# Kernel tuning notes

Hardware: AMD Instinct MI355X
Metric: run time of the kernel (lower is better)

Reference implementation:

```python
import jax, jax.numpy as jnp
import numpy as np

N, E, F_IN, H1, H2, C, K, G = 50000, 800000, 64, 64, 128, 2, 5, 64


def setup_inputs() -> dict:
    key = jax.random.key(0)
    ks = jax.random.split(key, 12)
    x = jax.random.normal(ks[0], (N, F_IN), dtype=jnp.float32)
    edge_index = jax.random.randint(ks[1], (2, E), 0, N, dtype=jnp.int64)
    edge_attr = jax.random.uniform(ks[2], (E,), dtype=jnp.float32)
    batch = jnp.sort(jax.random.randint(ks[3], (N,), 0, G, dtype=jnp.int64))
    def glorot(k, shape, fan_in):
        return jax.random.normal(k, shape, dtype=jnp.float32) * (1.0 / np.sqrt(fan_in))
    # ChebConv weights: [K, in, out]
    W1 = glorot(ks[4], (K, F_IN, H1), F_IN)
    b1 = jnp.zeros((H1,), jnp.float32)
    W2 = glorot(ks[5], (K, H1, H1), H1)
    b2 = jnp.zeros((H1,), jnp.float32)
    W3 = glorot(ks[6], (K, H1, H2), H1)
    b3 = jnp.zeros((H2,), jnp.float32)
    Wl = glorot(ks[7], (H2, C), H2)
    bl = jnp.zeros((C,), jnp.float32)
    return {"x": x, "edge_index": edge_index, "edge_attr": edge_attr, "batch": batch,
            "W1": W1, "b1": b1, "W2": W2, "b2": b2, "W3": W3, "b3": b3, "Wl": Wl, "bl": bl}


def _cheb_norm(edge_index, edge_attr, num_nodes):
    # sym-normalized scaled Laplacian L_hat = 2L/lambda_max - I with lambda_max=2:
    # off-diagonal weights -D^{-1/2} A D^{-1/2}; diagonal is exactly 0.
    src = edge_index[0]
    dst = edge_index[1]
    deg = jax.ops.segment_sum(edge_attr, src, num_segments=num_nodes)
    dis = jnp.where(deg > 0, jax.lax.rsqrt(deg), 0.0)
    norm = -dis[src] * edge_attr * dis[dst]
    return src, dst, norm


def _cheb_conv(x, src, dst, norm, W, b):
    # out = sum_k T_k(L_hat) x @ W[k], Chebyshev recurrence T_k = 2 L_hat T_{k-1} - T_{k-2}
    num_nodes = x.shape[0]
    def prop(z):  # L_hat @ z via edge gather-scale-scatter
        return jax.ops.segment_sum(norm[:, None] * z[src], dst, num_segments=num_nodes)
    Kk = W.shape[0]
    Tx0 = x
    out = Tx0 @ W[0]
    if Kk > 1:
        Tx1 = prop(Tx0)
        out = out + Tx1 @ W[1]
        for k in range(2, Kk):
            Tx2 = 2.0 * prop(Tx1) - Tx0
            out = out + Tx2 @ W[k]
            Tx0, Tx1 = Tx1, Tx2
    return out + b


def reference(x, edge_index, edge_attr, batch, W1, b1, W2, b2, W3, b3, Wl, bl):
    num_nodes = x.shape[0]
    src, dst, norm = _cheb_norm(edge_index, edge_attr, num_nodes)
    h = jax.nn.relu(_cheb_conv(x, src, dst, norm, W1, b1))
    h = jax.nn.relu(_cheb_conv(h, src, dst, norm, W2, b2))
    h = jax.nn.relu(_cheb_conv(h, src, dst, norm, W3, b3))
    # global mean pool over graph segment ids
    sums = jax.ops.segment_sum(h, batch, num_segments=G)
    cnt = jax.ops.segment_sum(jnp.ones((num_nodes,), h.dtype), batch, num_segments=G)
    hg = sums / jnp.maximum(cnt, 1.0)[:, None]
    out = hg @ Wl + bl
    return (out, hg)
```

## Files before the change

kernel.cpp:

```cpp
#include <hip/hip_runtime.h>
#include <hip/hip_fp16.h>


constexpr int F = 64;
constexpr int H2C = 128;
constexpr int GG = 64;
constexpr int CC = 2;
constexpr int KT = 5;
constexpr int PP = 16;

typedef __attribute__((ext_vector_type(8))) short short8v;
typedef __attribute__((ext_vector_type(4))) float f32x4;
typedef unsigned short ushortT;
typedef __attribute__((ext_vector_type(4))) unsigned short u16x4;
typedef __attribute__((ext_vector_type(8))) unsigned short u16x8;

__device__ inline ushortT f2bf(float f) {
  unsigned u = __float_as_uint(f);
  u = (u + 0x7fffu + ((u >> 16) & 1u)) >> 16;
  return (ushortT)u;
}
__device__ inline float bf2f(ushortT u) {
  return __uint_as_float((unsigned)u << 16);
}
__device__ inline float h2f_bits(unsigned short b) {
  __half_raw hr; hr.x = b;
  return __half2float(*reinterpret_cast<__half*>(&hr));
}
__device__ inline unsigned short f2h_bits(float v) {
  __half h = __float2half(v);
  return reinterpret_cast<__half_raw*>(&h)->x;
}


__global__ void pre_hist(const int* __restrict__ ei, const float* __restrict__ attr,
                         float* __restrict__ deg, int* __restrict__ cnt,
                         ushortT* __restrict__ rankr, int E) {
  int e = blockIdx.x * 256 + threadIdx.x;
  if (e < E) {
    atomicAdd(&deg[ei[e]], attr[e]);
    int rk = atomicAdd(&cnt[ei[E + e]], 1);
    rankr[e] = (ushortT)rk;
  }
}

__global__ void dis_k(const float* __restrict__ deg, float* __restrict__ dis, int n) {
  int i = blockIdx.x * 256 + threadIdx.x;
  if (i < n) { float d = deg[i]; dis[i] = d > 0.f ? rsqrtf(d) : 0.f; }
}


__global__ __launch_bounds__(256) void scan_a(const int* __restrict__ cnt,
                                              int* __restrict__ bsum, int n) {
  int t = threadIdx.x, lane = t & 63, w = t >> 6;
  int base = blockIdx.x * 1024 + t * 4;
  int s = 0;
#pragma unroll
  for (int j = 0; j < 4; ++j) { int i = base + j; if (i < n) s += cnt[i]; }
#pragma unroll
  for (int d = 1; d < 64; d <<= 1) s += __shfl_down(s, d, 64);
  __shared__ int ws[4];
  if (lane == 0) ws[w] = s;
  __syncthreads();
  if (t == 0) bsum[blockIdx.x] = ws[0] + ws[1] + ws[2] + ws[3];
}

__global__ void scan_b(int* __restrict__ bsum, int nb) {
  if (threadIdx.x == 0) {
    int acc = 0;
    for (int i = 0; i < nb; ++i) { acc += bsum[i]; bsum[i] = acc; }
  }
}

__global__ __launch_bounds__(256) void scan_c(const int* __restrict__ cnt,
                                              const int* __restrict__ bscan,
                                              int* __restrict__ off, int n) {
  int b = blockIdx.x, t = threadIdx.x;
  int lane = t & 63, w = t >> 6;
  int idx = b * 1024 + t * 4;
  int v[4];
#pragma unroll
  for (int j = 0; j < 4; ++j) { int i = idx + j; v[j] = (i < n) ? cnt[i] : 0; }
  int s1 = v[0], s2 = s1 + v[1], s3 = s2 + v[2], s4 = s3 + v[3];
  int x = s4;
#pragma unroll
  for (int d = 1; d < 64; d <<= 1) { int y = __shfl_up(x, d, 64); if (lane >= d) x += y; }
  __shared__ int wtot[4];
  if (lane == 63) wtot[w] = x;
  __syncthreads();
  int wbase = 0;
  for (int i = 0; i < w; ++i) wbase += wtot[i];
  int base = ((b > 0) ? bscan[b - 1] : 0) + wbase + (x - s4);
  if (idx + 0 < n) off[idx + 1] = base + s1;
  if (idx + 1 < n) off[idx + 2] = base + s2;
  if (idx + 2 < n) off[idx + 3] = base + s3;
  if (idx + 3 < n) off[idx + 4] = base + s4;
  if (b == 0 && t == 0) off[0] = 0;
}

__global__ void scatter_k(const int* __restrict__ ei, const float* __restrict__ attr,
                          const float* __restrict__ dis,
                          const ushortT* __restrict__ rankr,
                          const int* __restrict__ off, unsigned* __restrict__ ep4,
                          int E) {
  int e = blockIdx.x * 256 + threadIdx.x;
  if (e < E) {
    int s = ei[e], d = ei[E + e];
    int pos = off[d] + (int)rankr[e];
    float nv = -dis[s] * attr[e] * dis[d];
    ep4[pos] = ((unsigned)f2h_bits(nv) << 16) | (unsigned)(s & 0xFFFF);
  }
}

__global__ void cvt_k(const float* __restrict__ x, ushortT* __restrict__ o, int n4) {
  int i = blockIdx.x * 256 + threadIdx.x;
  if (i < n4) {
    float4 v = ((const float4*)x)[i];
    u16x4 r = {f2bf(v.x), f2bf(v.y), f2bf(v.z), f2bf(v.w)};
    ((u16x4*)o)[i] = r;
  }
}


__global__ __launch_bounds__(256) void prop_k(const ushortT* __restrict__ z,
                                              const int* __restrict__ off,
                                              const unsigned* __restrict__ ep4,
                                              const float* __restrict__ TprevF,
                                              const ushortT* __restrict__ TprevB,
                                              ushortT* __restrict__ out_bf, int n) {
  int wid = (blockIdx.x * 256 + threadIdx.x) >> 6;
  int lane = threadIdx.x & 63;
  if (wid >= n) return;
  int s = off[wid], e = off[wid + 1];
  int sub = lane & 7;
  int t = lane >> 3;
  float acc[8];
#pragma unroll
  for (int c = 0; c < 8; ++c) acc[c] = 0.f;
  for (int base = s; base < e; base += 64) {
    int idx = base + lane;
    unsigned m = (idx < e) ? ep4[idx] : 0u;
    int cntc = min(64, e - base);
    for (int j = 0; j < cntc; j += 16) {
      unsigned me0 = (unsigned)__shfl((int)m, j + t, 64);
      unsigned me1 = (unsigned)__shfl((int)m, j + 8 + t, 64);
      float w0 = h2f_bits((unsigned short)(me0 >> 16));
      float w1 = h2f_bits((unsigned short)(me1 >> 16));
      int s0 = (int)(me0 & 0xFFFF);
      int s1 = (int)(me1 & 0xFFFF);
      u16x8 v0 = *(const u16x8*)(z + ((size_t)s0 << 6) + sub * 8);
      u16x8 v1 = *(const u16x8*)(z + ((size_t)s1 << 6) + sub * 8);
#pragma unroll
      for (int c = 0; c < 8; ++c) acc[c] = fmaf(w0, bf2f(v0[c]), acc[c]);
#pragma unroll
      for (int c = 0; c < 8; ++c) acc[c] = fmaf(w1, bf2f(v1[c]), acc[c]);
    }
  }
#pragma unroll
  for (int c = 0; c < 8; ++c) {
    float v = acc[c];
    v += __shfl_xor(v, 8, 64);
    v += __shfl_xor(v, 16, 64);
    v += __shfl_xor(v, 32, 64);
    acc[c] = v;
  }
  if (lane < 8) {
    size_t oi = ((size_t)wid << 6) + (size_t)lane * 8;
    float r[8];
    if (TprevF) {
      const float4* tp = (const float4*)(TprevF + oi);
      float4 t0 = tp[0], t1 = tp[1];
      r[0] = 2.f * acc[0] - t0.x; r[1] = 2.f * acc[1] - t0.y;
      r[2] = 2.f * acc[2] - t0.z; r[3] = 2.f * acc[3] - t0.w;
      r[4] = 2.f * acc[4] - t1.x; r[5] = 2.f * acc[5] - t1.y;
      r[6] = 2.f * acc[6] - t1.z; r[7] = 2.f * acc[7] - t1.w;
    } else if (TprevB) {
      u16x8 tp = *(const u16x8*)(TprevB + oi);
#pragma unroll
      for (int c = 0; c < 8; ++c) r[c] = 2.f * acc[c] - bf2f(tp[c]);
    } else {
#pragma unroll
      for (int c = 0; c < 8; ++c) r[c] = acc[c];
    }
    u16x8 o;
#pragma unroll
    for (int c = 0; c < 8; ++c) o[c] = f2bf(r[c]);
    *(u16x8*)(out_bf + oi) = o;
  }
}


__global__ void repack_k(const float* __restrict__ W, ushortT* __restrict__ Bp, int H) {
  int t = blockIdx.x * 256 + threadIdx.x;
  int lane = t & 63, fid = t >> 6;
  int CT = H / 16;
  int nf = KT * 2 * CT;
  if (fid >= nf) return;
  int ct = fid % CT;
  int ks = (fid / CT) & 1;
  int term = fid / (CT * 2);
  int nn = ct * 16 + (lane & 15);
  int kb = ks * 32 + (lane >> 4) * 8;
  short8v out;
#pragma unroll
  for (int e = 0; e < 8; ++e)
    out[e] = (short)f2bf(W[((size_t)term * F + kb + e) * H + nn]);
  ((short8v*)Bp)[(size_t)fid * 64 + lane] = out;
}


template <int H>
__global__ __launch_bounds__(256) void gemm5_mfma(const ushortT* __restrict__ T0,
                                                  const ushortT* __restrict__ T1,
                                                  const ushortT* __restrict__ T2,
                                                  const ushortT* __restrict__ T3,
                                                  const ushortT* __restrict__ T4,
                                                  const ushortT* __restrict__ Bp,
                                                  const float* __restrict__ bias,
                                                  ushortT* __restrict__ Y, int n) {
  constexpr int CT = H / 16;
  int wave = threadIdx.x >> 6;
  int lane = threadIdx.x & 63;
  int rbase = blockIdx.x * 64 + wave * 16;
  int arow = rbase + (lane & 15);
  if (arow > n - 1) arow = n - 1;
  const short8v* bp = (const short8v*)Bp;
  const ushortT* Ts[5] = {T0, T1, T2, T3, T4};

  f32x4 acc[CT];
#pragma unroll
  for (int c = 0; c < CT; ++c) acc[c] = (f32x4){0.f, 0.f, 0.f, 0.f};

#pragma unroll
  for (int term = 0; term < KT; ++term) {
    const ushortT* T = Ts[term];
#pragma unroll
    for (int ks = 0; ks < 2; ++ks) {
      int kb = ks * 32 + (lane >> 4) * 8;
      short8v af = *(const short8v*)(T + (size_t)arow * F + kb);
      int fid0 = (term * 2 + ks) * CT;
#pragma unroll
      for (int ct = 0; ct < CT; ++ct) {
        short8v bf = bp[(size_t)(fid0 + ct) * 64 + lane];
        acc[ct] = __builtin_amdgcn_mfma_f32_16x16x32_bf16(af, bf, acc[ct], 0, 0, 0);
      }
    }
  }
  int col0 = lane & 15;
  int rrow = rbase + (lane >> 4) * 4;
#pragma unroll
  for (int ct = 0; ct < CT; ++ct) {
    int col = ct * 16 + col0;
    float bv = bias[col];
#pragma unroll
    for (int i = 0; i < 4; ++i) {
      int gr = rrow + i;
      if (gr < n) Y[(size_t)gr * H + col] = f2bf(fmaxf(acc[ct][i] + bv, 0.f));
    }
  }
}


__global__ void gbounds_k(const int* __restrict__ batch, int* __restrict__ gstart, int n) {
  int g = threadIdx.x;
  if (g > GG) return;
  int lo = 0, hi = n;
  while (lo < hi) {
    int mid = (lo + hi) >> 1;
    if (batch[mid] < g) lo = mid + 1; else hi = mid;
  }
  gstart[g] = lo;
}

__global__ __launch_bounds__(256) void pool1_k(const ushortT* __restrict__ h,
                                               const int* __restrict__ gstart,
                                               float* __restrict__ partials) {
  int g = blockIdx.x / PP, p = blockIdx.x % PP;
  int s = gstart[g], e = gstart[g + 1];
  int len = e - s;
  int ss = s + (int)((long long)len * p / PP);
  int se = s + (int)((long long)len * (p + 1) / PP);
  int tid = threadIdx.x;
  int c = tid & (H2C - 1), half = tid >> 7;
  float acc = 0.f;
  for (int i = ss + half; i < se; i += 2)
    acc += bf2f(h[(size_t)i * H2C + c]);
  __shared__ float sums[2][H2C];
  sums[half][c] = acc;
  __syncthreads();
  if (tid < H2C)
    partials[(size_t)blockIdx.x * H2C + tid] = sums[0][tid] + sums[1][tid];
}

__global__ __launch_bounds__(128) void pool2_k(const float* __restrict__ partials,
                                               const int* __restrict__ gstart,
                                               const float* __restrict__ Wl,
                                               const float* __restrict__ bl,
                                               float* __restrict__ outp) {
  int g = blockIdx.x, tid = threadIdx.x;
  float s = 0.f;
  for (int p = 0; p < PP; ++p) s += partials[(size_t)(g * PP + p) * H2C + tid];
  float cntv = fmaxf((float)(gstart[g + 1] - gstart[g]), 1.f);
  float hg = s / cntv;
  outp[GG * CC + g * H2C + tid] = hg;
  __shared__ float red[2][H2C];
  red[0][tid] = hg * Wl[tid * CC + 0];
  red[1][tid] = hg * Wl[tid * CC + 1];
  __syncthreads();
  for (int st = 64; st > 0; st >>= 1) {
    if (tid < st) { red[0][tid] += red[0][tid + st]; red[1][tid] += red[1][tid + st]; }
    __syncthreads();
  }
  if (tid == 0) {
    outp[g * CC + 0] = red[0][0] + bl[0];
    outp[g * CC + 1] = red[1][0] + bl[1];
  }
}


extern "C" void kernel_launch(void* const* d_in, const int* in_sizes, int n_in,
                              void* d_out, int out_size, void* d_ws, size_t ws_size,
                              hipStream_t stream) {
  const float* x    = (const float*)d_in[0];
  const int*   ei   = (const int*)d_in[1];
  const float* attr = (const float*)d_in[2];
  const int*   batch= (const int*)d_in[3];
  const float* W1 = (const float*)d_in[4];
  const float* b1 = (const float*)d_in[5];
  const float* W2 = (const float*)d_in[6];
  const float* b2 = (const float*)d_in[7];
  const float* W3 = (const float*)d_in[8];
  const float* b3 = (const float*)d_in[9];
  const float* Wl = (const float*)d_in[10];
  const float* bl = (const float*)d_in[11];
  float* outp = (float*)d_out;

  const int N = in_sizes[3];
  const int E = in_sizes[2];

  char* p = (char*)d_ws;
  auto alloc = [&](size_t bytes) {
    char* r = p;
    p += (bytes + 255) & ~(size_t)255;
    return r;
  };
  float* deg   = (float*)alloc((size_t)N * 4);
  int*   cnt   = (int*)alloc((size_t)N * 4);
  float* dis   = (float*)alloc((size_t)N * 4);
  int*   off   = (int*)alloc((size_t)(N + 1) * 4);
  ushortT* rankr = (ushortT*)alloc((size_t)E * 2);
  unsigned* ep4 = (unsigned*)alloc((size_t)E * 4);
  int*   bsum  = (int*)alloc(4096);
  int*   gstart= (int*)alloc((size_t)(GG + 1) * 4);
  ushortT* Bp1 = (ushortT*)alloc((size_t)KT * 2 * 4 * 64 * 8 * 2);
  ushortT* Bp2 = (ushortT*)alloc((size_t)KT * 2 * 4 * 64 * 8 * 2);
  ushortT* Bp3 = (ushortT*)alloc((size_t)KT * 2 * 8 * 64 * 8 * 2);
  ushortT* X0  = (ushortT*)alloc((size_t)N * F * 2);
  ushortT* Abf = (ushortT*)alloc((size_t)N * F * 2);
  ushortT* Bbf = (ushortT*)alloc((size_t)N * F * 2);
  ushortT* Cbf = (ushortT*)alloc((size_t)N * F * 2);
  ushortT* Dbf = (ushortT*)alloc((size_t)N * F * 2);
  ushortT* Y1  = (ushortT*)alloc((size_t)N * F * 2);
  ushortT* Y2  = (ushortT*)alloc((size_t)N * F * 2);
  ushortT* Y3  = (ushortT*)alloc((size_t)N * H2C * 2);
  float* partials = (float*)alloc((size_t)GG * PP * H2C * 4);

  hipMemsetAsync(deg, 0, (size_t)N * 4, stream);
  hipMemsetAsync(cnt, 0, (size_t)N * 4, stream);

  int eb = (E + 255) / 256;
  int nb = (N + 255) / 256;
  int sb = (N + 1023) / 1024;

  repack_k<<<(KT * 2 * 4 * 64 + 255) / 256, 256, 0, stream>>>(W1, Bp1, 64);
  repack_k<<<(KT * 2 * 4 * 64 + 255) / 256, 256, 0, stream>>>(W2, Bp2, 64);
  repack_k<<<(KT * 2 * 8 * 64 + 255) / 256, 256, 0, stream>>>(W3, Bp3, 128);
  cvt_k<<<((N * F / 4) + 255) / 256, 256, 0, stream>>>(x, X0, N * F / 4);

  pre_hist<<<eb, 256, 0, stream>>>(ei, attr, deg, cnt, rankr, E);
  dis_k<<<nb, 256, 0, stream>>>(deg, dis, N);
  scan_a<<<sb, 256, 0, stream>>>(cnt, bsum, N);
  scan_b<<<1, 64, 0, stream>>>(bsum, sb);
  scan_c<<<sb, 256, 0, stream>>>(cnt, bsum, off, N);
  scatter_k<<<eb, 256, 0, stream>>>(ei, attr, dis, rankr, off, ep4, E);
  gbounds_k<<<1, 128, 0, stream>>>(batch, gstart, N);

  int pb = (N + 3) / 4;
  auto prop = [&](const ushortT* z, const float* TprevF, const ushortT* TprevB,
                  ushortT* obf) {
    prop_k<<<pb, 256, 0, stream>>>(z, off, ep4, TprevF, TprevB, obf, N);
  };

  auto run_layer = [&](const ushortT* T0, const float* T0f, const ushortT* Bpk,
                       const float* bk, ushortT* Yout, int Hout) {
    prop(T0, nullptr, nullptr, Abf);
    prop(Abf, T0f, T0f ? nullptr : T0, Bbf);
    prop(Bbf, nullptr, Abf, Cbf);
    prop(Cbf, nullptr, Bbf, Dbf);
    if (Hout == 64)
      gemm5_mfma<64><<<(N + 63) / 64, 256, 0, stream>>>(T0, Abf, Bbf, Cbf, Dbf,
                                                        Bpk, bk, Yout, N);
    else
      gemm5_mfma<128><<<(N + 63) / 64, 256, 0, stream>>>(T0, Abf, Bbf, Cbf, Dbf,
                                                         Bpk, bk, Yout, N);
  };

  run_layer(X0, x,       Bp1, b1, Y1, 64);
  run_layer(Y1, nullptr, Bp2, b2, Y2, 64);
  run_layer(Y2, nullptr, Bp3, b3, Y3, 128);

  pool1_k<<<GG * PP, 256, 0, stream>>>(Y3, gstart, partials);
  pool2_k<<<GG, 128, 0, stream>>>(partials, gstart, Wl, bl, outp);
}
```

Before: 452.9 us.

## Process four nodes per wave in prop with prefetched edge lists; hoist GEMM A loads

Result: no change. 453.9 us (+0.2%).

```diff
diff --git a/kernel.cpp b/kernel.cpp
--- a/kernel.cpp
+++ b/kernel.cpp
@@ -128,64 +128,89 @@
                                               const float* __restrict__ TprevF,
                                               const ushortT* __restrict__ TprevB,
                                               ushortT* __restrict__ out_bf, int n) {
-  int wid = (blockIdx.x * 256 + threadIdx.x) >> 6;
+  int wv = (blockIdx.x * 256 + threadIdx.x) >> 6;
   int lane = threadIdx.x & 63;
-  if (wid >= n) return;
-  int s = off[wid], e = off[wid + 1];
+  int n0 = wv * 4;
+  if (n0 >= n) return;
   int sub = lane & 7;
   int t = lane >> 3;
-  float acc[8];
-#pragma unroll
-  for (int c = 0; c < 8; ++c) acc[c] = 0.f;
-  for (int base = s; base < e; base += 64) {
-    int idx = base + lane;
-    unsigned m = (idx < e) ? ep4[idx] : 0u;
-    int cntc = min(64, e - base);
-    for (int j = 0; j < cntc; j += 16) {
-      unsigned me0 = (unsigned)__shfl((int)m, j + t, 64);
-      unsigned me1 = (unsigned)__shfl((int)m, j + 8 + t, 64);
-      float w0 = h2f_bits((unsigned short)(me0 >> 16));
-      float w1 = h2f_bits((unsigned short)(me1 >> 16));
-      int s0 = (int)(me0 & 0xFFFF);
-      int s1 = (int)(me1 & 0xFFFF);
-      u16x8 v0 = *(const u16x8*)(z + ((size_t)s0 << 6) + sub * 8);
-      u16x8 v1 = *(const u16x8*)(z + ((size_t)s1 << 6) + sub * 8);
-#pragma unroll
-      for (int c = 0; c < 8; ++c) acc[c] = fmaf(w0, bf2f(v0[c]), acc[c]);
-#pragma unroll
-      for (int c = 0; c < 8; ++c) acc[c] = fmaf(w1, bf2f(v1[c]), acc[c]);
-    }
-  }
-#pragma unroll
-  for (int c = 0; c < 8; ++c) {
-    float v = acc[c];
-    v += __shfl_xor(v, 8, 64);
-    v += __shfl_xor(v, 16, 64);
-    v += __shfl_xor(v, 32, 64);
-    acc[c] = v;
-  }
-  if (lane < 8) {
-    size_t oi = ((size_t)wid << 6) + (size_t)lane * 8;
-    float r[8];
-    if (TprevF) {
-      const float4* tp = (const float4*)(TprevF + oi);
-      float4 t0 = tp[0], t1 = tp[1];
-      r[0] = 2.f * acc[0] - t0.x; r[1] = 2.f * acc[1] - t0.y;
-      r[2] = 2.f * acc[2] - t0.z; r[3] = 2.f * acc[3] - t0.w;
-      r[4] = 2.f * acc[4] - t1.x; r[5] = 2.f * acc[5] - t1.y;
-      r[6] = 2.f * acc[6] - t1.z; r[7] = 2.f * acc[7] - t1.w;
-    } else if (TprevB) {
-      u16x8 tp = *(const u16x8*)(TprevB + oi);
-#pragma unroll
-      for (int c = 0; c < 8; ++c) r[c] = 2.f * acc[c] - bf2f(tp[c]);
-    } else {
-#pragma unroll
-      for (int c = 0; c < 8; ++c) r[c] = acc[c];
-    }
-    u16x8 o;
-#pragma unroll
-    for (int c = 0; c < 8; ++c) o[c] = f2bf(r[c]);
-    *(u16x8*)(out_bf + oi) = o;
+  int offv = 0;
+  {
+    int oi = n0 + lane;
+    if (lane <= 4 && oi <= n) offv = off[oi];
+  }
+  int s_i = __builtin_amdgcn_readlane(offv, 0);
+  int e_i = __builtin_amdgcn_readlane(offv, 1);
+  unsigned m_cur = (s_i + lane < e_i) ? ep4[s_i + lane] : 0u;
+
+#pragma unroll
+  for (int i = 0; i < 4; ++i) {
+    int nd = n0 + i;
+    if (nd >= n) break;
+    int s = s_i, e = e_i;
+    int s_n = 0, e_n = 0;
+    unsigned m_next = 0u;
+    if (i < 3) {
+      s_n = __builtin_amdgcn_readlane(offv, i + 1);
+      e_n = __builtin_amdgcn_readlane(offv, i + 2);
+      m_next = (s_n + lane < e_n) ? ep4[s_n + lane] : 0u;
+    }
+    float acc[8];
+#pragma unroll
+    for (int c = 0; c < 8; ++c) acc[c] = 0.f;
+    unsigned m = m_cur;
+    int base = s;
+    while (base < e) {
+      int cntc = min(64, e - base);
+      for (int j = 0; j < cntc; j += 16) {
+        unsigned me0 = (unsigned)__shfl((int)m, j + t, 64);
+        unsigned me1 = (unsigned)__shfl((int)m, j + 8 + t, 64);
+        float w0 = h2f_bits((unsigned short)(me0 >> 16));
+        float w1 = h2f_bits((unsigned short)(me1 >> 16));
+        int s0 = (int)(me0 & 0xFFFF);
+        int s1 = (int)(me1 & 0xFFFF);
+        u16x8 v0 = *(const u16x8*)(z + ((size_t)s0 << 6) + sub * 8);
+        u16x8 v1 = *(const u16x8*)(z + ((size_t)s1 << 6) + sub * 8);
+#pragma unroll
+        for (int c = 0; c < 8; ++c) acc[c] = fmaf(w0, bf2f(v0[c]), acc[c]);
+#pragma unroll
+        for (int c = 0; c < 8; ++c) acc[c] = fmaf(w1, bf2f(v1[c]), acc[c]);
+      }
+      base += 64;
+      if (base < e) m = (base + lane < e) ? ep4[base + lane] : 0u;
+    }
+#pragma unroll
+    for (int c = 0; c < 8; ++c) {
+      float v = acc[c];
+      v += __shfl_xor(v, 8, 64);
+      v += __shfl_xor(v, 16, 64);
+      v += __shfl_xor(v, 32, 64);
+      acc[c] = v;
+    }
+    if (lane < 8) {
+      size_t oi = ((size_t)nd << 6) + (size_t)lane * 8;
+      float r[8];
+      if (TprevF) {
+        const float4* tp = (const float4*)(TprevF + oi);
+        float4 t0 = tp[0], t1 = tp[1];
+        r[0] = 2.f * acc[0] - t0.x; r[1] = 2.f * acc[1] - t0.y;
+        r[2] = 2.f * acc[2] - t0.z; r[3] = 2.f * acc[3] - t0.w;
+        r[4] = 2.f * acc[4] - t1.x; r[5] = 2.f * acc[5] - t1.y;
+        r[6] = 2.f * acc[6] - t1.z; r[7] = 2.f * acc[7] - t1.w;
+      } else if (TprevB) {
+        u16x8 tp = *(const u16x8*)(TprevB + oi);
+#pragma unroll
+        for (int c = 0; c < 8; ++c) r[c] = 2.f * acc[c] - bf2f(tp[c]);
+      } else {
+#pragma unroll
+        for (int c = 0; c < 8; ++c) r[c] = acc[c];
+      }
+      u16x8 o;
+#pragma unroll
+      for (int c = 0; c < 8; ++c) o[c] = f2bf(r[c]);
+      *(u16x8*)(out_bf + oi) = o;
+    }
+    s_i = s_n; e_i = e_n; m_cur = m_next;
   }
 }
 
@@ -226,24 +251,27 @@
   if (arow > n - 1) arow = n - 1;
   const short8v* bp = (const short8v*)Bp;
   const ushortT* Ts[5] = {T0, T1, T2, T3, T4};
-
-  f32x4 acc[CT];
-#pragma unroll
-  for (int c = 0; c < CT; ++c) acc[c] = (f32x4){0.f, 0.f, 0.f, 0.f};
-
+  int kb = (lane >> 4) * 8;
+
+  short8v afr[10];
 #pragma unroll
   for (int term = 0; term < KT; ++term) {
     const ushortT* T = Ts[term];
-#pragma unroll
-    for (int ks = 0; ks < 2; ++ks) {
-      int kb = ks * 32 + (lane >> 4) * 8;
-      short8v af = *(const short8v*)(T + (size_t)arow * F + kb);
-      int fid0 = (term * 2 + ks) * CT;
-#pragma unroll
-      for (int ct = 0; ct < CT; ++ct) {
-        short8v bf = bp[(size_t)(fid0 + ct) * 64 + lane];
-        acc[ct] = __builtin_amdgcn_mfma_f32_16x16x32_bf16(af, bf, acc[ct], 0, 0, 0);
-      }
+    afr[term * 2 + 0] = *(const short8v*)(T + (size_t)arow * F + kb);
+    afr[term * 2 + 1] = *(const short8v*)(T + (size_t)arow * F + 32 + kb);
+  }
+
+  f32x4 acc[CT];
+#pragma unroll
+  for (int c = 0; c < CT; ++c) acc[c] = (f32x4){0.f, 0.f, 0.f, 0.f};
+
+#pragma unroll
+  for (int f = 0; f < KT * 2; ++f) {
+    short8v af = afr[f];
+#pragma unroll
+    for (int ct = 0; ct < CT; ++ct) {
+      short8v bf = bp[(size_t)(f * CT + ct) * 64 + lane];
+      acc[ct] = __builtin_amdgcn_mfma_f32_16x16x32_bf16(af, bf, acc[ct], 0, 0, 0);
     }
   }
   int col0 = lane & 15;
@@ -385,7 +413,7 @@
   scatter_k<<<eb, 256, 0, stream>>>(ei, attr, dis, rankr, off, ep4, E);
   gbounds_k<<<1, 128, 0, stream>>>(batch, gstart, N);
 
-  int pb = (N + 3) / 4;
+  int pb = (N + 15) / 16;
   auto prop = [&](const ushortT* z, const float* TprevF, const ushortT* TprevB,
                   ushortT* obf) {
     prop_k<<<pb, 256, 0, stream>>>(z, off, ep4, TprevF, TprevB, obf, N);
```

## Split feature matrices into two 32-column planes for cache-friendly propagation

Applied to the files above, without the earlier changes.

After: 654.3 us. 44.5% more time.

```diff
diff --git a/kernel.cpp b/kernel.cpp
--- a/kernel.cpp
+++ b/kernel.cpp
@@ -112,28 +112,42 @@
   }
 }
 
-__global__ void cvt_k(const float* __restrict__ x, ushortT* __restrict__ o, int n4) {
+__global__ void cvt_k(const float* __restrict__ x, ushortT* __restrict__ oa,
+                      ushortT* __restrict__ ob, int n) {
   int i = blockIdx.x * 256 + threadIdx.x;
-  if (i < n4) {
+  if (i < n * 16) {
+    int row = i >> 4;
+    int c4 = (i & 15) * 4;
     float4 v = ((const float4*)x)[i];
     u16x4 r = {f2bf(v.x), f2bf(v.y), f2bf(v.z), f2bf(v.w)};
-    ((u16x4*)o)[i] = r;
-  }
-}
-
-
-__global__ __launch_bounds__(256) void prop_k(const ushortT* __restrict__ z,
+    ushortT* dst = (c4 >= 32 ? ob : oa) + (size_t)row * 32 + (c4 & 31);
+    *(u16x4*)dst = r;
+  }
+}
+
+
+__global__ __launch_bounds__(256) void prop_k(const ushortT* __restrict__ z0,
+                                              const ushortT* __restrict__ z1,
                                               const int* __restrict__ off,
                                               const unsigned* __restrict__ ep4,
                                               const float* __restrict__ TprevF,
-                                              const ushortT* __restrict__ TprevB,
-                                              ushortT* __restrict__ out_bf, int n) {
-  int wid = (blockIdx.x * 256 + threadIdx.x) >> 6;
+                                              const ushortT* __restrict__ tb0,
+                                              const ushortT* __restrict__ tb1,
+                                              ushortT* __restrict__ o0,
+                                              ushortT* __restrict__ o1, int n) {
+  int bid = blockIdx.x;
+  int half = (bid >> 2) & 1;
+  int tile = (bid >> 3) * 4 + (bid & 3);
+  int wave = threadIdx.x >> 6;
   int lane = threadIdx.x & 63;
-  if (wid >= n) return;
-  int s = off[wid], e = off[wid + 1];
-  int sub = lane & 7;
-  int t = lane >> 3;
+  int nd = tile * 4 + wave;
+  if (nd >= n) return;
+  const ushortT* z = half ? z1 : z0;
+  const ushortT* tb = half ? tb1 : tb0;
+  ushortT* op = half ? o1 : o0;
+  int sub = lane & 3;
+  int t = lane >> 2;
+  int s = off[nd], e = off[nd + 1];
   float acc[8];
 #pragma unroll
   for (int c = 0; c < 8; ++c) acc[c] = 0.f;
@@ -142,40 +156,35 @@
     unsigned m = (idx < e) ? ep4[idx] : 0u;
     int cntc = min(64, e - base);
     for (int j = 0; j < cntc; j += 16) {
-      unsigned me0 = (unsigned)__shfl((int)m, j + t, 64);
-      unsigned me1 = (unsigned)__shfl((int)m, j + 8 + t, 64);
-      float w0 = h2f_bits((unsigned short)(me0 >> 16));
-      float w1 = h2f_bits((unsigned short)(me1 >> 16));
-      int s0 = (int)(me0 & 0xFFFF);
-      int s1 = (int)(me1 & 0xFFFF);
-      u16x8 v0 = *(const u16x8*)(z + ((size_t)s0 << 6) + sub * 8);
-      u16x8 v1 = *(const u16x8*)(z + ((size_t)s1 << 6) + sub * 8);
-#pragma unroll
-      for (int c = 0; c < 8; ++c) acc[c] = fmaf(w0, bf2f(v0[c]), acc[c]);
-#pragma unroll
-      for (int c = 0; c < 8; ++c) acc[c] = fmaf(w1, bf2f(v1[c]), acc[c]);
+      unsigned me = (unsigned)__shfl((int)m, j + t, 64);
+      float w = h2f_bits((unsigned short)(me >> 16));
+      int src = (int)(me & 0xFFFF);
+      u16x8 v = *(const u16x8*)(z + ((size_t)src << 5) + sub * 8);
+#pragma unroll
+      for (int c = 0; c < 8; ++c) acc[c] = fmaf(w, bf2f(v[c]), acc[c]);
     }
   }
 #pragma unroll
   for (int c = 0; c < 8; ++c) {
     float v = acc[c];
+    v += __shfl_xor(v, 4, 64);
     v += __shfl_xor(v, 8, 64);
     v += __shfl_xor(v, 16, 64);
     v += __shfl_xor(v, 32, 64);
     acc[c] = v;
   }
-  if (lane < 8) {
-    size_t oi = ((size_t)wid << 6) + (size_t)lane * 8;
+  if (lane < 4) {
+    size_t oi = ((size_t)nd << 5) + (size_t)lane * 8;
     float r[8];
     if (TprevF) {
-      const float4* tp = (const float4*)(TprevF + oi);
+      const float4* tp = (const float4*)(TprevF + ((size_t)nd << 6) + half * 32 + lane * 8);
       float4 t0 = tp[0], t1 = tp[1];
       r[0] = 2.f * acc[0] - t0.x; r[1] = 2.f * acc[1] - t0.y;
       r[2] = 2.f * acc[2] - t0.z; r[3] = 2.f * acc[3] - t0.w;
       r[4] = 2.f * acc[4] - t1.x; r[5] = 2.f * acc[5] - t1.y;
       r[6] = 2.f * acc[6] - t1.z; r[7] = 2.f * acc[7] - t1.w;
-    } else if (TprevB) {
-      u16x8 tp = *(const u16x8*)(TprevB + oi);
+    } else if (tb) {
+      u16x8 tp = *(const u16x8*)(tb + oi);
 #pragma unroll
       for (int c = 0; c < 8; ++c) r[c] = 2.f * acc[c] - bf2f(tp[c]);
     } else {
@@ -185,7 +194,7 @@
     u16x8 o;
 #pragma unroll
     for (int c = 0; c < 8; ++c) o[c] = f2bf(r[c]);
-    *(u16x8*)(out_bf + oi) = o;
+    *(u16x8*)(op + oi) = o;
   }
 }
 
@@ -210,14 +219,14 @@
 
 
 template <int H>
-__global__ __launch_bounds__(256) void gemm5_mfma(const ushortT* __restrict__ T0,
-                                                  const ushortT* __restrict__ T1,
-                                                  const ushortT* __restrict__ T2,
-                                                  const ushortT* __restrict__ T3,
-                                                  const ushortT* __restrict__ T4,
-                                                  const ushortT* __restrict__ Bp,
-                                                  const float* __restrict__ bias,
-                                                  ushortT* __restrict__ Y, int n) {
+__global__ __launch_bounds__(256) void gemm5_mfma(
+    const ushortT* __restrict__ T0a, const ushortT* __restrict__ T0b,
+    const ushortT* __restrict__ T1a, const ushortT* __restrict__ T1b,
+    const ushortT* __restrict__ T2a, const ushortT* __restrict__ T2b,
+    const ushortT* __restrict__ T3a, const ushortT* __restrict__ T3b,
+    const ushortT* __restrict__ T4a, const ushortT* __restrict__ T4b,
+    const ushortT* __restrict__ Bp, const float* __restrict__ bias,
+    ushortT* __restrict__ Ya, ushortT* __restrict__ Yb, int n) {
   constexpr int CT = H / 16;
   int wave = threadIdx.x >> 6;
   int lane = threadIdx.x & 63;
@@ -225,25 +234,28 @@
   int arow = rbase + (lane & 15);
   if (arow > n - 1) arow = n - 1;
   const short8v* bp = (const short8v*)Bp;
-  const ushortT* Ts[5] = {T0, T1, T2, T3, T4};
+  const ushortT* Tsa[5] = {T0a, T1a, T2a, T3a, T4a};
+  const ushortT* Tsb[5] = {T0b, T1b, T2b, T3b, T4b};
+  int kb8 = (lane >> 4) * 8;
+
+  short8v afr[10];
+#pragma unroll
+  for (int term = 0; term < KT; ++term) {
+    afr[term * 2 + 0] = *(const short8v*)(Tsa[term] + ((size_t)arow << 5) + kb8);
+    afr[term * 2 + 1] = *(const short8v*)(Tsb[term] + ((size_t)arow << 5) + kb8);
+  }
 
   f32x4 acc[CT];
 #pragma unroll
   for (int c = 0; c < CT; ++c) acc[c] = (f32x4){0.f, 0.f, 0.f, 0.f};
 
 #pragma unroll
-  for (int term = 0; term < KT; ++term) {
-    const ushortT* T = Ts[term];
-#pragma unroll
-    for (int ks = 0; ks < 2; ++ks) {
-      int kb = ks * 32 + (lane >> 4) * 8;
-      short8v af = *(const short8v*)(T + (size_t)arow * F + kb);
-      int fid0 = (term * 2 + ks) * CT;
-#pragma unroll
-      for (int ct = 0; ct < CT; ++ct) {
-        short8v bf = bp[(size_t)(fid0 + ct) * 64 + lane];
-        acc[ct] = __builtin_amdgcn_mfma_f32_16x16x32_bf16(af, bf, acc[ct], 0, 0, 0);
-      }
+  for (int f = 0; f < KT * 2; ++f) {
+    short8v af = afr[f];
+#pragma unroll
+    for (int ct = 0; ct < CT; ++ct) {
+      short8v bf = bp[(size_t)(f * CT + ct) * 64 + lane];
+      acc[ct] = __builtin_amdgcn_mfma_f32_16x16x32_bf16(af, bf, acc[ct], 0, 0, 0);
     }
   }
   int col0 = lane & 15;
@@ -255,7 +267,15 @@
 #pragma unroll
     for (int i = 0; i < 4; ++i) {
       int gr = rrow + i;
-      if (gr < n) Y[(size_t)gr * H + col] = f2bf(fmaxf(acc[ct][i] + bv, 0.f));
+      if (gr < n) {
+        ushortT v = f2bf(fmaxf(acc[ct][i] + bv, 0.f));
+        if (H == 128) {
+          Ya[(size_t)gr * H + col] = v;
+        } else {
+          ushortT* dst = (col >= 32 ? Yb : Ya);
+          dst[((size_t)gr << 5) + (col & 31)] = v;
+        }
+      }
     }
   }
 }
@@ -355,18 +375,19 @@
   ushortT* Bp1 = (ushortT*)alloc((size_t)KT * 2 * 4 * 64 * 8 * 2);
   ushortT* Bp2 = (ushortT*)alloc((size_t)KT * 2 * 4 * 64 * 8 * 2);
   ushortT* Bp3 = (ushortT*)alloc((size_t)KT * 2 * 8 * 64 * 8 * 2);
-  ushortT* X0  = (ushortT*)alloc((size_t)N * F * 2);
-  ushortT* Abf = (ushortT*)alloc((size_t)N * F * 2);
-  ushortT* Bbf = (ushortT*)alloc((size_t)N * F * 2);
-  ushortT* Cbf = (ushortT*)alloc((size_t)N * F * 2);
-  ushortT* Dbf = (ushortT*)alloc((size_t)N * F * 2);
-  ushortT* Y1  = (ushortT*)alloc((size_t)N * F * 2);
-  ushortT* Y2  = (ushortT*)alloc((size_t)N * F * 2);
+  size_t plane = (size_t)N * 32;
+  ushortT* X0a = (ushortT*)alloc(plane * 2); ushortT* X0b = (ushortT*)alloc(plane * 2);
+  ushortT* Aa  = (ushortT*)alloc(plane * 2); ushortT* Ab  = (ushortT*)alloc(plane * 2);
+  ushortT* Ba  = (ushortT*)alloc(plane * 2); ushortT* Bb  = (ushortT*)alloc(plane * 2);
+  ushortT* Ca  = (ushortT*)alloc(plane * 2); ushortT* Cb  = (ushortT*)alloc(plane * 2);
+  ushortT* Da  = (ushortT*)alloc(plane * 2); ushortT* Db  = (ushortT*)alloc(plane * 2);
+  ushortT* Y1a = (ushortT*)alloc(plane * 2); ushortT* Y1b = (ushortT*)alloc(plane * 2);
+  ushortT* Y2a = (ushortT*)alloc(plane * 2); ushortT* Y2b = (ushortT*)alloc(plane * 2);
   ushortT* Y3  = (ushortT*)alloc((size_t)N * H2C * 2);
   float* partials = (float*)alloc((size_t)GG * PP * H2C * 4);
 
-  hipMemsetAsync(deg, 0, (size_t)N * 4, stream);
-  hipMemsetAsync(cnt, 0, (size_t)N * 4, stream);
+  size_t degPad = ((size_t)N * 4 + 255) & ~(size_t)255;
+  hipMemsetAsync(deg, 0, degPad + (size_t)N * 4, stream);
 
   int eb = (E + 255) / 256;
   int nb = (N + 255) / 256;
@@ -375,7 +396,7 @@
   repack_k<<<(KT * 2 * 4 * 64 + 255) / 256, 256, 0, stream>>>(W1, Bp1, 64);
   repack_k<<<(KT * 2 * 4 * 64 + 255) / 256, 256, 0, stream>>>(W2, Bp2, 64);
   repack_k<<<(KT * 2 * 8 * 64 + 255) / 256, 256, 0, stream>>>(W3, Bp3, 128);
-  cvt_k<<<((N * F / 4) + 255) / 256, 256, 0, stream>>>(x, X0, N * F / 4);
+  cvt_k<<<((N * 16) + 255) / 256, 256, 0, stream>>>(x, X0a, X0b, N);
 
   pre_hist<<<eb, 256, 0, stream>>>(ei, attr, deg, cnt, rankr, E);
   dis_k<<<nb, 256, 0, stream>>>(deg, dis, N);
@@ -385,29 +406,33 @@
   scatter_k<<<eb, 256, 0, stream>>>(ei, attr, dis, rankr, off, ep4, E);
   gbounds_k<<<1, 128, 0, stream>>>(batch, gstart, N);
 
-  int pb = (N + 3) / 4;
-  auto prop = [&](const ushortT* z, const float* TprevF, const ushortT* TprevB,
-                  ushortT* obf) {
-    prop_k<<<pb, 256, 0, stream>>>(z, off, ep4, TprevF, TprevB, obf, N);
+  int ntiles = (N + 3) / 4;
+  int ntp = ((ntiles + 3) / 4) * 4;
+  int pgrid = 2 * ntp;
+  auto prop = [&](const ushortT* za, const ushortT* zb, const float* TprevF,
+                  const ushortT* tba, const ushortT* tbb,
+                  ushortT* oa, ushortT* ob) {
+    prop_k<<<pgrid, 256, 0, stream>>>(za, zb, off, ep4, TprevF, tba, tbb, oa, ob, N);
   };
 
-  auto run_layer = [&](const ushortT* T0, const float* T0f, const ushortT* Bpk,
-                       const float* bk, ushortT* Yout, int Hout) {
-    prop(T0, nullptr, nullptr, Abf);
-    prop(Abf, T0f, T0f ? nullptr : T0, Bbf);
-    prop(Bbf, nullptr, Abf, Cbf);
-    prop(Cbf, nullptr, Bbf, Dbf);
+  auto run_layer = [&](const ushortT* T0a, const ushortT* T0b, const float* T0f,
+                       const ushortT* Bpk, const float* bk,
+                       ushortT* Yla, ushortT* Ylb, int Hout) {
+    prop(T0a, T0b, nullptr, nullptr, nullptr, Aa, Ab);
+    prop(Aa, Ab, T0f, T0f ? nullptr : T0a, T0f ? nullptr : T0b, Ba, Bb);
+    prop(Ba, Bb, nullptr, Aa, Ab, Ca, Cb);
+    prop(Ca, Cb, nullptr, Ba, Bb, Da, Db);
     if (Hout == 64)
-      gemm5_mfma<64><<<(N + 63) / 64, 256, 0, stream>>>(T0, Abf, Bbf, Cbf, Dbf,
-                                                        Bpk, bk, Yout, N);
+      gemm5_mfma<64><<<(N + 63) / 64, 256, 0, stream>>>(
+          T0a, T0b, Aa, Ab, Ba, Bb, Ca, Cb, Da, Db, Bpk, bk, Yla, Ylb, N);
     else
-      gemm5_mfma<128><<<(N + 63) / 64, 256, 0, stream>>>(T0, Abf, Bbf, Cbf, Dbf,
-                                                         Bpk, bk, Yout, N);
+      gemm5_mfma<128><<<(N + 63) / 64, 256, 0, stream>>>(
+          T0a, T0b, Aa, Ab, Ba, Bb, Ca, Cb, Da, Db, Bpk, bk, Yla, nullptr, N);
   };
 
-  run_layer(X0, x,       Bp1, b1, Y1, 64);
-  run_layer(Y1, nullptr, Bp2, b2, Y2, 64);
-  run_layer(Y2, nullptr, Bp3, b3, Y3, 128);
+  run_layer(X0a, X0b, x,       Bp1, b1, Y1a, Y1b, 64);
+  run_layer(Y1a, Y1b, nullptr, Bp2, b2, Y2a, Y2b, 64);
+  run_layer(Y2a, Y2b, nullptr, Bp3, b3, Y3, nullptr, 128);
 
   pool1_k<<<GG * PP, 256, 0, stream>>>(Y3, gstart, partials);
   pool2_k<<<GG, 128, 0, stream>>>(partials, gstart, Wl, bl, outp);
```

## Replace global-atomic degree histogram with per-block packed LDS histograms and merge

Applied to the files above, without the earlier changes.

Result: no change. 453.1 us (+0.0%).

```diff
diff --git a/kernel.cpp b/kernel.cpp
--- a/kernel.cpp
+++ b/kernel.cpp
@@ -8,6 +8,9 @@
 constexpr int CC = 2;
 constexpr int KT = 5;
 constexpr int PP = 16;
+constexpr int EPB = 8192;
+constexpr int NQ = 12500;
+constexpr int QW = NQ / 2;
 
 typedef __attribute__((ext_vector_type(8))) short short8v;
 typedef __attribute__((ext_vector_type(4))) float f32x4;
@@ -33,20 +36,68 @@
 }
 
 
-__global__ void pre_hist(const int* __restrict__ ei, const float* __restrict__ attr,
-                         float* __restrict__ deg, int* __restrict__ cnt,
-                         ushortT* __restrict__ rankr, int E) {
-  int e = blockIdx.x * 256 + threadIdx.x;
-  if (e < E) {
-    atomicAdd(&deg[ei[e]], attr[e]);
-    int rk = atomicAdd(&cnt[ei[E + e]], 1);
-    rankr[e] = (ushortT)rk;
-  }
-}
-
-__global__ void dis_k(const float* __restrict__ deg, float* __restrict__ dis, int n) {
-  int i = blockIdx.x * 256 + threadIdx.x;
-  if (i < n) { float d = deg[i]; dis[i] = d > 0.f ? rsqrtf(d) : 0.f; }
+__global__ __launch_bounds__(256) void hist_k(const int* __restrict__ ei,
+                                              const float* __restrict__ attr,
+                                              unsigned* __restrict__ degP,
+                                              unsigned* __restrict__ cntP,
+                                              ushortT* __restrict__ lrank, int E) {
+  __shared__ unsigned hd[QW];
+  __shared__ unsigned hc[QW];
+  int blk = blockIdx.x, tid = threadIdx.x;
+  int e0 = blk * EPB;
+#pragma unroll 1
+  for (int q = 0; q < 4; ++q) {
+    int nbase = q * NQ;
+    for (int i = tid; i < QW; i += 256) { hd[i] = 0u; hc[i] = 0u; }
+    __syncthreads();
+    for (int i = tid; i < EPB; i += 256) {
+      int e = e0 + i;
+      if (e < E) {
+        int s = ei[e], d = ei[E + e];
+        if ((unsigned)(s - nbase) < (unsigned)NQ) {
+          unsigned fv = (unsigned)__float2uint_rn(attr[e] * 512.f);
+          int sl = s - nbase;
+          atomicAdd(&hd[sl >> 1], fv << (16 * (sl & 1)));
+        }
+        if ((unsigned)(d - nbase) < (unsigned)NQ) {
+          int dl = d - nbase;
+          unsigned old = atomicAdd(&hc[dl >> 1], 1u << (16 * (dl & 1)));
+          lrank[e] = (ushortT)((old >> (16 * (dl & 1))) & 0xFFFFu);
+        }
+      }
+    }
+    __syncthreads();
+    for (int i = tid; i < QW; i += 256) {
+      degP[(size_t)blk * (4 * QW) + q * QW + i] = hd[i];
+      cntP[(size_t)blk * (4 * QW) + q * QW + i] = hc[i];
+    }
+    __syncthreads();
+  }
+}
+
+__global__ __launch_bounds__(256) void merge_k(const unsigned* __restrict__ degP,
+                                               const unsigned* __restrict__ cntP,
+                                               float* __restrict__ dis,
+                                               int* __restrict__ cnt,
+                                               unsigned char* __restrict__ planeoff,
+                                               int nb, int nwords, int N) {
+  int w = blockIdx.x * 256 + threadIdx.x;
+  if (w >= nwords) return;
+  unsigned sd0 = 0, sd1 = 0, c0 = 0, c1 = 0;
+  for (int p = 0; p < nb; ++p) {
+    unsigned dv = degP[(size_t)p * nwords + w];
+    unsigned cv = cntP[(size_t)p * nwords + w];
+    unsigned short pk = (unsigned short)((c0 & 0xFFu) | ((c1 & 0xFFu) << 8));
+    *(unsigned short*)(planeoff + (size_t)p * N + 2 * w) = pk;
+    sd0 += dv & 0xFFFFu; sd1 += dv >> 16;
+    c0 += cv & 0xFFFFu;  c1 += cv >> 16;
+  }
+  float d0 = (float)sd0 * (1.f / 512.f);
+  float d1 = (float)sd1 * (1.f / 512.f);
+  dis[2 * w]     = d0 > 0.f ? rsqrtf(d0) : 0.f;
+  dis[2 * w + 1] = d1 > 0.f ? rsqrtf(d1) : 0.f;
+  cnt[2 * w]     = (int)c0;
+  cnt[2 * w + 1] = (int)c1;
 }
 
 
@@ -100,13 +151,15 @@
 
 __global__ void scatter_k(const int* __restrict__ ei, const float* __restrict__ attr,
                           const float* __restrict__ dis,
-                          const ushortT* __restrict__ rankr,
-                          const int* __restrict__ off, unsigned* __restrict__ ep4,
-                          int E) {
+                          const ushortT* __restrict__ lrank,
+                          const int* __restrict__ off,
+                          const unsigned char* __restrict__ planeoff,
+                          unsigned* __restrict__ ep4, int E, int N) {
   int e = blockIdx.x * 256 + threadIdx.x;
   if (e < E) {
     int s = ei[e], d = ei[E + e];
-    int pos = off[d] + (int)rankr[e];
+    int b = e >> 13;
+    int pos = off[d] + (int)planeoff[(size_t)b * N + d] + (int)lrank[e];
     float nv = -dis[s] * attr[e] * dis[d];
     ep4[pos] = ((unsigned)f2h_bits(nv) << 16) | (unsigned)(s & 0xFFFF);
   }
@@ -190,22 +243,27 @@
 }
 
 
-__global__ void repack_k(const float* __restrict__ W, ushortT* __restrict__ Bp, int H) {
+__global__ void repack3_k(const float* __restrict__ W1, const float* __restrict__ W2,
+                          const float* __restrict__ W3, ushortT* __restrict__ Bp1,
+                          ushortT* __restrict__ Bp2, ushortT* __restrict__ Bp3) {
   int t = blockIdx.x * 256 + threadIdx.x;
   int lane = t & 63, fid = t >> 6;
+  const float* W; ushortT* Bp; int H; int f;
+  if (fid < 40)       { W = W1; Bp = Bp1; H = 64;  f = fid; }
+  else if (fid < 80)  { W = W2; Bp = Bp2; H = 64;  f = fid - 40; }
+  else if (fid < 160) { W = W3; Bp = Bp3; H = 128; f = fid - 80; }
+  else return;
   int CT = H / 16;
-  int nf = KT * 2 * CT;
-  if (fid >= nf) return;
-  int ct = fid % CT;
-  int ks = (fid / CT) & 1;
-  int term = fid / (CT * 2);
+  int ct = f % CT;
+  int ks = (f / CT) & 1;
+  int term = f / (CT * 2);
   int nn = ct * 16 + (lane & 15);
   int kb = ks * 32 + (lane >> 4) * 8;
   short8v out;
 #pragma unroll
   for (int e = 0; e < 8; ++e)
     out[e] = (short)f2bf(W[((size_t)term * F + kb + e) * H + nn]);
-  ((short8v*)Bp)[(size_t)fid * 64 + lane] = out;
+  ((short8v*)Bp)[(size_t)f * 64 + lane] = out;
 }
 
 
@@ -226,24 +284,27 @@
   if (arow > n - 1) arow = n - 1;
   const short8v* bp = (const short8v*)Bp;
   const ushortT* Ts[5] = {T0, T1, T2, T3, T4};
-
-  f32x4 acc[CT];
-#pragma unroll
-  for (int c = 0; c < CT; ++c) acc[c] = (f32x4){0.f, 0.f, 0.f, 0.f};
-
+  int kb = (lane >> 4) * 8;
+
+  short8v afr[10];
 #pragma unroll
   for (int term = 0; term < KT; ++term) {
     const ushortT* T = Ts[term];
-#pragma unroll
-    for (int ks = 0; ks < 2; ++ks) {
-      int kb = ks * 32 + (lane >> 4) * 8;
-      short8v af = *(const short8v*)(T + (size_t)arow * F + kb);
-      int fid0 = (term * 2 + ks) * CT;
-#pragma unroll
-      for (int ct = 0; ct < CT; ++ct) {
-        short8v bf = bp[(size_t)(fid0 + ct) * 64 + lane];
-        acc[ct] = __builtin_amdgcn_mfma_f32_16x16x32_bf16(af, bf, acc[ct], 0, 0, 0);
-      }
+    afr[term * 2 + 0] = *(const short8v*)(T + (size_t)arow * F + kb);
+    afr[term * 2 + 1] = *(const short8v*)(T + (size_t)arow * F + 32 + kb);
+  }
+
+  f32x4 acc[CT];
+#pragma unroll
+  for (int c = 0; c < CT; ++c) acc[c] = (f32x4){0.f, 0.f, 0.f, 0.f};
+
+#pragma unroll
+  for (int f = 0; f < KT * 2; ++f) {
+    short8v af = afr[f];
+#pragma unroll
+    for (int ct = 0; ct < CT; ++ct) {
+      short8v bf = bp[(size_t)(f * CT + ct) * 64 + lane];
+      acc[ct] = __builtin_amdgcn_mfma_f32_16x16x32_bf16(af, bf, acc[ct], 0, 0, 0);
     }
   }
   int col0 = lane & 15;
@@ -337,6 +398,8 @@
 
   const int N = in_sizes[3];
   const int E = in_sizes[2];
+  const int NB = (E + EPB - 1) / EPB;
+  const int NW = 4 * QW;
 
   char* p = (char*)d_ws;
   auto alloc = [&](size_t bytes) {
@@ -344,12 +407,14 @@
     p += (bytes + 255) & ~(size_t)255;
     return r;
   };
-  float* deg   = (float*)alloc((size_t)N * 4);
+  float* dis   = (float*)alloc((size_t)N * 4);
   int*   cnt   = (int*)alloc((size_t)N * 4);
-  float* dis   = (float*)alloc((size_t)N * 4);
   int*   off   = (int*)alloc((size_t)(N + 1) * 4);
-  ushortT* rankr = (ushortT*)alloc((size_t)E * 2);
+  ushortT* lrank = (ushortT*)alloc((size_t)E * 2);
   unsigned* ep4 = (unsigned*)alloc((size_t)E * 4);
+  unsigned* degP = (unsigned*)alloc((size_t)NB * NW * 4);
+  unsigned* cntP = (unsigned*)alloc((size_t)NB * NW * 4);
+  unsigned char* planeoff = (unsigned char*)alloc((size_t)NB * N);
   int*   bsum  = (int*)alloc(4096);
   int*   gstart= (int*)alloc((size_t)(GG + 1) * 4);
   ushortT* Bp1 = (ushortT*)alloc((size_t)KT * 2 * 4 * 64 * 8 * 2);
@@ -365,24 +430,19 @@
   ushortT* Y3  = (ushortT*)alloc((size_t)N * H2C * 2);
   float* partials = (float*)alloc((size_t)GG * PP * H2C * 4);
 
-  hipMemsetAsync(deg, 0, (size_t)N * 4, stream);
-  hipMemsetAsync(cnt, 0, (size_t)N * 4, stream);
-
   int eb = (E + 255) / 256;
-  int nb = (N + 255) / 256;
   int sb = (N + 1023) / 1024;
 
-  repack_k<<<(KT * 2 * 4 * 64 + 255) / 256, 256, 0, stream>>>(W1, Bp1, 64);
-  repack_k<<<(KT * 2 * 4 * 64 + 255) / 256, 256, 0, stream>>>(W2, Bp2, 64);
-  repack_k<<<(KT * 2 * 8 * 64 + 255) / 256, 256, 0, stream>>>(W3, Bp3, 128);
+  repack3_k<<<40, 256, 0, stream>>>(W1, W2, W3, Bp1, Bp2, Bp3);
   cvt_k<<<((N * F / 4) + 255) / 256, 256, 0, stream>>>(x, X0, N * F / 4);
 
-  pre_hist<<<eb, 256, 0, stream>>>(ei, attr, deg, cnt, rankr, E);
-  dis_k<<<nb, 256, 0, stream>>>(deg, dis, N);
+  hist_k<<<NB, 256, 0, stream>>>(ei, attr, degP, cntP, lrank, E);
+  merge_k<<<(NW + 255) / 256, 256, 0, stream>>>(degP, cntP, dis, cnt, planeoff,
+                                                NB, NW, N);
   scan_a<<<sb, 256, 0, stream>>>(cnt, bsum, N);
   scan_b<<<1, 64, 0, stream>>>(bsum, sb);
   scan_c<<<sb, 256, 0, stream>>>(cnt, bsum, off, N);
-  scatter_k<<<eb, 256, 0, stream>>>(ei, attr, dis, rankr, off, ep4, E);
+  scatter_k<<<eb, 256, 0, stream>>>(ei, attr, dis, lrank, off, planeoff, ep4, E, N);
   gbounds_k<<<1, 128, 0, stream>>>(batch, gstart, N);
 
   int pb = (N + 3) / 4;
```
